# Optimization experiments

Hardware: AMD Instinct MI355X
Metric: run time of the kernel (lower is better)

Reference implementation:

```python
import jax, jax.numpy as jnp
import numpy as np


def _ste(x, q):
    # straight-through estimator: forward=q, backward=identity
    return x + jax.lax.stop_gradient(q - x)


def quant_act_int8(x, s):
    # Int8 per-tensor fake-quant: clamp(round(x/s), -128, 127) * s
    q = jnp.clip(jnp.round(x / s), -128.0, 127.0) * s
    return _ste(x, q)


def binarize_weight(w):
    # BINARY weight quant: scale * sign(w), scale = mean(|w|) per tensor (STE)
    s = jnp.mean(jnp.abs(jax.lax.stop_gradient(w)))
    return _ste(w, s * jnp.sign(w))


def setup_inputs() -> dict:
    key = jax.random.key(0)
    ks = jax.random.split(key, 7)
    B, D_IN, H, D_OUT = 65536, 784, 128, 10
    f32 = jnp.float32
    return {
        "input_tensor": jax.random.normal(ks[0], (B, D_IN), f32),
        "w1": jax.random.normal(ks[1], (D_IN, H), f32) * 0.05,
        "b1": jnp.zeros((H,), f32),
        "w2": jax.random.normal(ks[2], (H, H), f32) * 0.05,
        "b2": jnp.zeros((H,), f32),
        "w3": jax.random.normal(ks[3], (H, D_OUT), f32) * 0.05,
        "b3": jnp.zeros((D_OUT,), f32),
        # learned per-tensor activation scales (Int8ActPerTensorFloat)
        "s_in": jnp.float32(0.03),
        "s1i": jnp.float32(0.05), "s1o": jnp.float32(0.05),
        "s2i": jnp.float32(0.05), "s2o": jnp.float32(0.05),
        "s3i": jnp.float32(0.05), "s3o": jnp.float32(0.01),
    }


def reference(input_tensor, w1, b1, w2, b2, w3, b3,
              s_in, s1i, s1o, s2i, s2o, s3i, s3o):
    hidden = []
    # quantize_input (QuantIdentity, int8 per-tensor)
    x = quant_act_int8(input_tensor, s_in)
    hidden.append(x)
    # input_layer: binary QuantLinear + bias, then QuantReLU (input_quant + act_quant)
    x = x @ binarize_weight(w1) + b1
    x = quant_act_int8(x, s1i)
    x = quant_act_int8(jax.nn.relu(x), s1o)
    hidden.append(x)
    # hidden_layer
    x = x @ binarize_weight(w2) + b2
    x = quant_act_int8(x, s2i)
    x = quant_act_int8(jax.nn.relu(x), s2o)
    hidden.append(x)
    # output_layer: binary QuantLinear then QuantSigmoid
    x = x @ binarize_weight(w3) + b3
    x = quant_act_int8(x, s3i)
    x = quant_act_int8(jax.nn.sigmoid(x), s3o)
    hidden.append(x)
    return (x, *hidden)
```

## Files before the change

kernel.cpp:

```cpp
#include <hip/hip_runtime.h>
#include <math.h>

typedef __bf16 bf16x8 __attribute__((ext_vector_type(8)));
typedef float f32x4 __attribute__((ext_vector_type(4)));
typedef unsigned short u16;
typedef u16 u16x8 __attribute__((ext_vector_type(8)));

__device__ __forceinline__ float quantq_inv(float x, float inv) {
    return fminf(fmaxf(rintf(x * inv), -128.f), 127.f);
}

__device__ __forceinline__ u16 sign_bf16(float w) {
    return (w > 0.f) ? (u16)0x3F80 : ((w < 0.f) ? (u16)0xBF80 : (u16)0);
}

__global__ void alpha_part(const float* __restrict__ w1,
                           const float* __restrict__ w2,
                           const float* __restrict__ w3,
                           float* __restrict__ partial) {
    __shared__ float red[256];
    const int bid = blockIdx.x;
    const int m = bid >> 5, i = bid & 31;
    const float* w = (m == 0) ? w1 : ((m == 1) ? w2 : w3);
    const int n = (m == 0) ? 100352 : ((m == 1) ? 16384 : 1280);
    const int chunk = n >> 5;
    const float* p = w + i * chunk;
    float s = 0.f;
    for (int t = threadIdx.x; t < chunk; t += 256) s += fabsf(p[t]);
    red[threadIdx.x] = s;
    __syncthreads();
    for (int off = 128; off > 0; off >>= 1) {
        if ((int)threadIdx.x < off) red[threadIdx.x] += red[threadIdx.x + off];
        __syncthreads();
    }
    if (threadIdx.x == 0) partial[bid] = red[0];
}

__global__ void alpha_final(const float* __restrict__ partial,
                            float* __restrict__ alphas) {
    const int t = threadIdx.x;
    if (t < 3) {
        float s = 0.f;
        for (int i = 0; i < 32; ++i) s += partial[t * 32 + i];
        const int n = (t == 0) ? 100352 : ((t == 1) ? 16384 : 1280);
        alphas[t] = s / (float)n;
    }
}

__global__ void pack_kernel(const float* __restrict__ w1,
                            const float* __restrict__ w2,
                            const float* __restrict__ w3,
                            u16* __restrict__ Wb1) {
    u16* Wb2 = Wb1 + 102400;
    u16* Wb3 = Wb2 + 16384;
    int idx = blockIdx.x * 256 + threadIdx.x;
    if (idx < 102400) {
        int k = idx >> 7, n = idx & 127;
        u16 v = (k < 784) ? sign_bf16(w1[k * 128 + n]) : (u16)0;
        int dest = ((((k >> 5) * 8 + (n >> 4)) * 64) + ((((k & 31) >> 3) << 4) | (n & 15))) * 8 + (k & 7);
        Wb1[dest] = v;
    } else if (idx < 102400 + 16384) {
        int i = idx - 102400;
        int k = i >> 7, n = i & 127;
        u16 v = sign_bf16(w2[k * 128 + n]);
        int dest = ((((k >> 5) * 8 + (n >> 4)) * 64) + ((((k & 31) >> 3) << 4) | (n & 15))) * 8 + (k & 7);
        Wb2[dest] = v;
    } else if (idx < 102400 + 16384 + 2048) {
        int i = idx - 102400 - 16384;
        int k = i >> 4, n = i & 15;
        u16 v = (n < 10) ? sign_bf16(w3[k * 10 + n]) : (u16)0;
        int dest = (((k >> 5) * 64) + ((((k & 31) >> 3) << 4) | n)) * 8 + (k & 7);
        Wb3[dest] = v;
    }
}

__global__ __launch_bounds__(256) void fused_kernel(
    const float* __restrict__ input,
    const float* __restrict__ bias1, const float* __restrict__ bias2,
    const float* __restrict__ bias3,
    const float* __restrict__ ps_in, const float* __restrict__ ps1i,
    const float* __restrict__ ps1o, const float* __restrict__ ps2i,
    const float* __restrict__ ps2o, const float* __restrict__ ps3i,
    const float* __restrict__ ps3o,
    const float* __restrict__ alphas, const u16* __restrict__ Wb1,
    float* __restrict__ out0, float* __restrict__ h0, float* __restrict__ h1,
    float* __restrict__ h2, float* __restrict__ h3)
{
    const u16* Wb2 = Wb1 + 102400;
    const u16* Wb3 = Wb2 + 16384;

    __shared__ u16 A2[8192];

    const int tid = threadIdx.x;
    const int wave = tid >> 6, lane = tid & 63;
    const int row0 = blockIdx.x * 64;

    const float s_in = *ps_in, s1i = *ps1i, s1o = *ps1o;
    const float s2i = *ps2i, s2o = *ps2o, s3i = *ps3i, s3o = *ps3o;
    const float inv_sin = 1.f / s_in, inv_s1i = 1.f / s1i, inv_s1o = 1.f / s1o;
    const float inv_s2i = 1.f / s2i, inv_s2o = 1.f / s2o;
    const float inv_s3i = 1.f / s3i, inv_s3o = 1.f / s3o;
    const float alpha1 = alphas[0], alpha2 = alphas[1], alpha3 = alphas[2];

    const int rA = lane & 15;
    const int gA = lane >> 4;
    const size_t arow = (size_t)(row0 + wave * 16 + rA) * 784;

    f32x4 acc1[8];
#pragma unroll
    for (int n = 0; n < 8; ++n) acc1[n] = f32x4{0.f, 0.f, 0.f, 0.f};

    f32x4 pv0, pv1;
    {
        const float* p = input + arow + gA * 8;
        pv0 = *reinterpret_cast<const f32x4*>(p);
        pv1 = *reinterpret_cast<const f32x4*>(p + 4);
    }
    const u16* bw1 = Wb1 + (size_t)lane * 8;

    for (int ksq = 0; ksq < 25; ++ksq) {
        float v[8];
#pragma unroll
        for (int j = 0; j < 4; ++j) { v[j] = pv0[j]; v[4 + j] = pv1[j]; }
        const bool valid = (ksq < 24) || (gA < 2);

        if (ksq < 24) {
            const int cb = (ksq + 1) * 32 + gA * 8;
            if (cb + 8 <= 784) {
                const float* p = input + arow + cb;
                pv0 = *reinterpret_cast<const f32x4*>(p);
                pv1 = *reinterpret_cast<const f32x4*>(p + 4);
            }
        }

        u16x8 qb;
        if (valid) {
            float q[8];
#pragma unroll
            for (int j = 0; j < 8; ++j) q[j] = quantq_inv(v[j], inv_sin);
            f32x4 ha = {q[0] * s_in, q[1] * s_in, q[2] * s_in, q[3] * s_in};
            f32x4 hb = {q[4] * s_in, q[5] * s_in, q[6] * s_in, q[7] * s_in};
            float* hp = h0 + arow + ksq * 32 + gA * 8;
            __builtin_nontemporal_store(ha, reinterpret_cast<f32x4*>(hp));
            __builtin_nontemporal_store(hb, reinterpret_cast<f32x4*>(hp + 4));
#pragma unroll
            for (int j = 0; j < 8; ++j) qb[j] = (u16)(__float_as_uint(q[j]) >> 16);
        } else {
#pragma unroll
            for (int j = 0; j < 8; ++j) qb[j] = (u16)0;
        }
        union { u16x8 u; bf16x8 b; } cvt;
        cvt.u = qb;
        const bf16x8 a = cvt.b;

        const u16* bp = bw1 + (size_t)ksq * 4096;
#pragma unroll
        for (int n = 0; n < 8; ++n) {
            const bf16x8 b = *reinterpret_cast<const bf16x8*>(bp + n * 512);
            acc1[n] = __builtin_amdgcn_mfma_f32_16x16x32_bf16(a, b, acc1[n], 0, 0, 0);
        }
    }

    const int cl = lane & 15;
    const int rh = lane >> 4;
    {
        const float a1s = alpha1 * s_in;
#pragma unroll
        for (int n = 0; n < 8; ++n) {
            const int col = n * 16 + cl;
            const float bias = bias1[col];
            const int ks = n >> 1;
            const int gk = ((n & 1) * 2) + (cl >> 3);
            const int jd = cl & 7;
#pragma unroll
            for (int j = 0; j < 4; ++j) {
                const int rl = rh * 4 + j;
                float x = a1s * acc1[n][j] + bias;
                x = quantq_inv(x, inv_s1i) * s1i;
                x = fmaxf(x, 0.f);
                const float qv = quantq_inv(x, inv_s1o);
                __builtin_nontemporal_store(qv * s1o,
                    h1 + (size_t)(row0 + wave * 16 + rl) * 128 + col);
                A2[(((ks * 4 + wave) * 64) + (gk * 16 + rl)) * 8 + jd] =
                    (u16)(__float_as_uint(qv) >> 16);
            }
        }
    }

    f32x4 acc2[8];
#pragma unroll
    for (int n = 0; n < 8; ++n) acc2[n] = f32x4{0.f, 0.f, 0.f, 0.f};
#pragma unroll
    for (int ks = 0; ks < 4; ++ks) {
        const bf16x8 a = *reinterpret_cast<const bf16x8*>(&A2[((ks * 4 + wave) * 64 + lane) * 8]);
#pragma unroll
        for (int n = 0; n < 8; ++n) {
            const bf16x8 b = *reinterpret_cast<const bf16x8*>(Wb2 + ((size_t)(ks * 8 + n) * 64 + lane) * 8);
            acc2[n] = __builtin_amdgcn_mfma_f32_16x16x32_bf16(a, b, acc2[n], 0, 0, 0);
        }
    }

    {
        const float a2s = alpha2 * s1o;
#pragma unroll
        for (int n = 0; n < 8; ++n) {
            const int col = n * 16 + cl;
            const float bias = bias2[col];
            const int ks = n >> 1;
            const int gk = ((n & 1) * 2) + (cl >> 3);
            const int jd = cl & 7;
#pragma unroll
            for (int j = 0; j < 4; ++j) {
                const int rl = rh * 4 + j;
                float x = a2s * acc2[n][j] + bias;
                x = quantq_inv(x, inv_s2i) * s2i;
                x = fmaxf(x, 0.f);
                const float qv = quantq_inv(x, inv_s2o);
                __builtin_nontemporal_store(qv * s2o,
                    h2 + (size_t)(row0 + wave * 16 + rl) * 128 + col);
                A2[(((ks * 4 + wave) * 64) + (gk * 16 + rl)) * 8 + jd] =
                    (u16)(__float_as_uint(qv) >> 16);
            }
        }
    }

    f32x4 acc3 = f32x4{0.f, 0.f, 0.f, 0.f};
#pragma unroll
    for (int ks = 0; ks < 4; ++ks) {
        const bf16x8 a = *reinterpret_cast<const bf16x8*>(&A2[((ks * 4 + wave) * 64 + lane) * 8]);
        const bf16x8 b = *reinterpret_cast<const bf16x8*>(Wb3 + ((size_t)ks * 64 + lane) * 8);
        acc3 = __builtin_amdgcn_mfma_f32_16x16x32_bf16(a, b, acc3, 0, 0, 0);
    }

    if (cl < 10) {
        const float a3s = alpha3 * s2o;
        const float bias = bias3[cl];
#pragma unroll
        for (int j = 0; j < 4; ++j) {
            const int rgl = row0 + wave * 16 + rh * 4 + j;
            float x = a3s * acc3[j] + bias;
            x = quantq_inv(x, inv_s3i) * s3i;
            const float sg = 1.f / (1.f + expf(-x));
            const float qv = quantq_inv(sg, inv_s3o) * s3o;
            out0[(size_t)rgl * 10 + cl] = qv;
            h3[(size_t)rgl * 10 + cl] = qv;
        }
    }
}

extern "C" void kernel_launch(void* const* d_in, const int* in_sizes, int n_in,
                              void* d_out, int out_size, void* d_ws, size_t ws_size,
                              hipStream_t stream) {
    const float* input = (const float*)d_in[0];
    const float* w1    = (const float*)d_in[1];
    const float* bias1 = (const float*)d_in[2];
    const float* w2    = (const float*)d_in[3];
    const float* bias2 = (const float*)d_in[4];
    const float* w3    = (const float*)d_in[5];
    const float* bias3 = (const float*)d_in[6];
    const float* s_in  = (const float*)d_in[7];
    const float* s1i   = (const float*)d_in[8];
    const float* s1o   = (const float*)d_in[9];
    const float* s2i   = (const float*)d_in[10];
    const float* s2o   = (const float*)d_in[11];
    const float* s3i   = (const float*)d_in[12];
    const float* s3o   = (const float*)d_in[13];

    float* out = (float*)d_out;
    float* out0 = out;
    float* h0 = out + 655360;
    float* h1 = out + 52035584;
    float* h2 = out + 60424192;
    float* h3 = out + 68812800;

    float* alphas  = (float*)d_ws;
    float* partial = (float*)((char*)d_ws + 16);
    u16*   Wb1     = (u16*)((char*)d_ws + 512);

    alpha_part<<<96, 256, 0, stream>>>(w1, w2, w3, partial);
    alpha_final<<<1, 64, 0, stream>>>(partial, alphas);
    pack_kernel<<<472, 256, 0, stream>>>(w1, w2, w3, Wb1);
    fused_kernel<<<1024, 256, 0, stream>>>(input, bias1, bias2, bias3,
                                           s_in, s1i, s1o, s2i, s2o, s3i, s3o,
                                           alphas, Wb1,
                                           out0, h0, h1, h2, h3);
}
```

Before: 122.0 us.

## Split layer-1 K loop across two wave groups and merge alpha_final into pack

Doubles the fused kernel block to 512 threads. Two groups of four waves each handle half of the 784-wide K dimension of the first GEMM, with two-deep register prefetch of the input, and their partial accumulators are reduced through shared memory before the second half of the block exits. The goal is more memory-level parallelism and latency hiding on the input read, which dominates the kernel. The alpha_final launch is folded into pack_kernel to save one launch. The cost is extra shared memory, three block barriers, and half the threads sitting idle for layers 2 and 3.

```diff
diff --git a/kernel.cpp b/kernel.cpp
--- a/kernel.cpp
+++ b/kernel.cpp
@@ -36,21 +36,19 @@
     if (threadIdx.x == 0) partial[bid] = red[0];
 }
 
-__global__ void alpha_final(const float* __restrict__ partial,
+__global__ void pack_kernel(const float* __restrict__ w1,
+                            const float* __restrict__ w2,
+                            const float* __restrict__ w3,
+                            u16* __restrict__ Wb1,
+                            const float* __restrict__ partial,
                             float* __restrict__ alphas) {
-    const int t = threadIdx.x;
-    if (t < 3) {
+    if (blockIdx.x == 0 && threadIdx.x < 3) {
+        const int t = threadIdx.x;
         float s = 0.f;
         for (int i = 0; i < 32; ++i) s += partial[t * 32 + i];
         const int n = (t == 0) ? 100352 : ((t == 1) ? 16384 : 1280);
         alphas[t] = s / (float)n;
     }
-}
-
-__global__ void pack_kernel(const float* __restrict__ w1,
-                            const float* __restrict__ w2,
-                            const float* __restrict__ w3,
-                            u16* __restrict__ Wb1) {
     u16* Wb2 = Wb1 + 102400;
     u16* Wb3 = Wb2 + 16384;
     int idx = blockIdx.x * 256 + threadIdx.x;
@@ -74,7 +72,7 @@
     }
 }
 
-__global__ __launch_bounds__(256) void fused_kernel(
+__global__ __launch_bounds__(512, 8) void fused_kernel(
     const float* __restrict__ input,
     const float* __restrict__ bias1, const float* __restrict__ bias2,
     const float* __restrict__ bias3,
@@ -89,10 +87,12 @@
     const u16* Wb2 = Wb1 + 102400;
     const u16* Wb3 = Wb2 + 16384;
 
+    __shared__ f32x4 Xch[1024];
     __shared__ u16 A2[8192];
 
     const int tid = threadIdx.x;
     const int wave = tid >> 6, lane = tid & 63;
+    const int wq = wave & 3, khalf = wave >> 2;
     const int row0 = blockIdx.x * 64;
 
     const float s_in = *ps_in, s1i = *ps1i, s1o = *ps1o;
@@ -104,62 +104,105 @@
 
     const int rA = lane & 15;
     const int gA = lane >> 4;
-    const size_t arow = (size_t)(row0 + wave * 16 + rA) * 784;
+    const size_t arow = (size_t)(row0 + wq * 16 + rA) * 784;
+    const float* __restrict__ inA = input + arow + gA * 8;
+    float* __restrict__ h0A = h0 + arow + gA * 8;
+    const u16* bw1 = Wb1 + (size_t)lane * 8;
 
     f32x4 acc1[8];
 #pragma unroll
     for (int n = 0; n < 8; ++n) acc1[n] = f32x4{0.f, 0.f, 0.f, 0.f};
 
-    f32x4 pv0, pv1;
-    {
-        const float* p = input + arow + gA * 8;
-        pv0 = *reinterpret_cast<const f32x4*>(p);
-        pv1 = *reinterpret_cast<const f32x4*>(p + 4);
-    }
-    const u16* bw1 = Wb1 + (size_t)lane * 8;
-
-    for (int ksq = 0; ksq < 25; ++ksq) {
-        float v[8];
-#pragma unroll
-        for (int j = 0; j < 4; ++j) { v[j] = pv0[j]; v[4 + j] = pv1[j]; }
-        const bool valid = (ksq < 24) || (gA < 2);
-
-        if (ksq < 24) {
-            const int cb = (ksq + 1) * 32 + gA * 8;
-            if (cb + 8 <= 784) {
-                const float* p = input + arow + cb;
-                pv0 = *reinterpret_cast<const f32x4*>(p);
-                pv1 = *reinterpret_cast<const f32x4*>(p + 4);
-            }
-        }
-
-        u16x8 qb;
-        if (valid) {
-            float q[8];
-#pragma unroll
-            for (int j = 0; j < 8; ++j) q[j] = quantq_inv(v[j], inv_sin);
+    auto consume = [&](int ksq, f32x4 va, f32x4 vb, bool dostore) {
+        float q[8];
+#pragma unroll
+        for (int j = 0; j < 4; ++j) {
+            q[j]     = quantq_inv(va[j], inv_sin);
+            q[4 + j] = quantq_inv(vb[j], inv_sin);
+        }
+        if (dostore) {
             f32x4 ha = {q[0] * s_in, q[1] * s_in, q[2] * s_in, q[3] * s_in};
             f32x4 hb = {q[4] * s_in, q[5] * s_in, q[6] * s_in, q[7] * s_in};
-            float* hp = h0 + arow + ksq * 32 + gA * 8;
+            float* hp = h0A + ksq * 32;
             __builtin_nontemporal_store(ha, reinterpret_cast<f32x4*>(hp));
             __builtin_nontemporal_store(hb, reinterpret_cast<f32x4*>(hp + 4));
-#pragma unroll
-            for (int j = 0; j < 8; ++j) qb[j] = (u16)(__float_as_uint(q[j]) >> 16);
-        } else {
-#pragma unroll
-            for (int j = 0; j < 8; ++j) qb[j] = (u16)0;
-        }
+        }
+        u16x8 qb;
+#pragma unroll
+        for (int j = 0; j < 8; ++j) qb[j] = (u16)(__float_as_uint(q[j]) >> 16);
         union { u16x8 u; bf16x8 b; } cvt;
         cvt.u = qb;
         const bf16x8 a = cvt.b;
-
         const u16* bp = bw1 + (size_t)ksq * 4096;
 #pragma unroll
         for (int n = 0; n < 8; ++n) {
             const bf16x8 b = *reinterpret_cast<const bf16x8*>(bp + n * 512);
             acc1[n] = __builtin_amdgcn_mfma_f32_16x16x32_bf16(a, b, acc1[n], 0, 0, 0);
         }
-    }
+    };
+
+    if (khalf == 0) {
+        f32x4 pa = *reinterpret_cast<const f32x4*>(inA + 0);
+        f32x4 pb = *reinterpret_cast<const f32x4*>(inA + 4);
+        f32x4 qa = *reinterpret_cast<const f32x4*>(inA + 32);
+        f32x4 qb = *reinterpret_cast<const f32x4*>(inA + 36);
+#pragma unroll
+        for (int k = 0; k < 12; ++k) {
+            f32x4 na = pa, nb = pb;
+            if (k + 2 < 12) {
+                na = *reinterpret_cast<const f32x4*>(inA + (k + 2) * 32);
+                nb = *reinterpret_cast<const f32x4*>(inA + (k + 2) * 32 + 4);
+            }
+            consume(k, pa, pb, true);
+            pa = qa; pb = qb; qa = na; qb = nb;
+        }
+    } else {
+        f32x4 pa = *reinterpret_cast<const f32x4*>(inA + 12 * 32);
+        f32x4 pb = *reinterpret_cast<const f32x4*>(inA + 12 * 32 + 4);
+        f32x4 qa = *reinterpret_cast<const f32x4*>(inA + 13 * 32);
+        f32x4 qb = *reinterpret_cast<const f32x4*>(inA + 13 * 32 + 4);
+#pragma unroll
+        for (int k = 0; k < 13; ++k) {
+            const int ksq = 12 + k;
+            const int t = ksq + 2;
+            f32x4 na, nb;
+            if (t < 24) {
+                na = *reinterpret_cast<const f32x4*>(inA + t * 32);
+                nb = *reinterpret_cast<const f32x4*>(inA + t * 32 + 4);
+            } else if (t == 24) {
+                if (gA < 2) {
+                    na = *reinterpret_cast<const f32x4*>(inA + 768);
+                    nb = *reinterpret_cast<const f32x4*>(inA + 768 + 4);
+                } else {
+                    na = f32x4{0.f, 0.f, 0.f, 0.f};
+                    nb = f32x4{0.f, 0.f, 0.f, 0.f};
+                }
+            } else {
+                na = pa; nb = pb;
+            }
+            consume(ksq, pa, pb, (ksq < 24) || (gA < 2));
+            pa = qa; pb = qb; qa = na; qb = nb;
+        }
+    }
+
+    if (khalf == 1) {
+#pragma unroll
+        for (int n = 0; n < 4; ++n) Xch[(wq * 4 + n) * 64 + lane] = acc1[n];
+    }
+    __syncthreads();
+    if (khalf == 0) {
+#pragma unroll
+        for (int n = 0; n < 4; ++n) acc1[n] += Xch[(wq * 4 + n) * 64 + lane];
+    }
+    __syncthreads();
+    if (khalf == 1) {
+#pragma unroll
+        for (int n = 0; n < 4; ++n) Xch[(wq * 4 + n) * 64 + lane] = acc1[4 + n];
+    }
+    __syncthreads();
+    if (khalf == 1) return;
+#pragma unroll
+    for (int n = 0; n < 4; ++n) acc1[4 + n] += Xch[(wq * 4 + n) * 64 + lane];
 
     const int cl = lane & 15;
     const int rh = lane >> 4;
@@ -180,8 +223,8 @@
                 x = fmaxf(x, 0.f);
                 const float qv = quantq_inv(x, inv_s1o);
                 __builtin_nontemporal_store(qv * s1o,
-                    h1 + (size_t)(row0 + wave * 16 + rl) * 128 + col);
-                A2[(((ks * 4 + wave) * 64) + (gk * 16 + rl)) * 8 + jd] =
+                    h1 + (size_t)(row0 + wq * 16 + rl) * 128 + col);
+                A2[(((ks * 4 + wq) * 64) + (gk * 16 + rl)) * 8 + jd] =
                     (u16)(__float_as_uint(qv) >> 16);
             }
         }
@@ -192,7 +235,7 @@
     for (int n = 0; n < 8; ++n) acc2[n] = f32x4{0.f, 0.f, 0.f, 0.f};
 #pragma unroll
     for (int ks = 0; ks < 4; ++ks) {
-        const bf16x8 a = *reinterpret_cast<const bf16x8*>(&A2[((ks * 4 + wave) * 64 + lane) * 8]);
+        const bf16x8 a = *reinterpret_cast<const bf16x8*>(&A2[((ks * 4 + wq) * 64 + lane) * 8]);
 #pragma unroll
         for (int n = 0; n < 8; ++n) {
             const bf16x8 b = *reinterpret_cast<const bf16x8*>(Wb2 + ((size_t)(ks * 8 + n) * 64 + lane) * 8);
@@ -217,8 +260,8 @@
                 x = fmaxf(x, 0.f);
                 const float qv = quantq_inv(x, inv_s2o);
                 __builtin_nontemporal_store(qv * s2o,
-                    h2 + (size_t)(row0 + wave * 16 + rl) * 128 + col);
-                A2[(((ks * 4 + wave) * 64) + (gk * 16 + rl)) * 8 + jd] =
+                    h2 + (size_t)(row0 + wq * 16 + rl) * 128 + col);
+                A2[(((ks * 4 + wq) * 64) + (gk * 16 + rl)) * 8 + jd] =
                     (u16)(__float_as_uint(qv) >> 16);
             }
         }
@@ -227,7 +270,7 @@
     f32x4 acc3 = f32x4{0.f, 0.f, 0.f, 0.f};
 #pragma unroll
     for (int ks = 0; ks < 4; ++ks) {
-        const bf16x8 a = *reinterpret_cast<const bf16x8*>(&A2[((ks * 4 + wave) * 64 + lane) * 8]);
+        const bf16x8 a = *reinterpret_cast<const bf16x8*>(&A2[((ks * 4 + wq) * 64 + lane) * 8]);
         const bf16x8 b = *reinterpret_cast<const bf16x8*>(Wb3 + ((size_t)ks * 64 + lane) * 8);
         acc3 = __builtin_amdgcn_mfma_f32_16x16x32_bf16(a, b, acc3, 0, 0, 0);
     }
@@ -237,7 +280,7 @@
         const float bias = bias3[cl];
 #pragma unroll
         for (int j = 0; j < 4; ++j) {
-            const int rgl = row0 + wave * 16 + rh * 4 + j;
+            const int rgl = row0 + wq * 16 + rh * 4 + j;
             float x = a3s * acc3[j] + bias;
             x = quantq_inv(x, inv_s3i) * s3i;
             const float sg = 1.f / (1.f + expf(-x));
@@ -278,9 +321,8 @@
     u16*   Wb1     = (u16*)((char*)d_ws + 512);
 
     alpha_part<<<96, 256, 0, stream>>>(w1, w2, w3, partial);
-    alpha_final<<<1, 64, 0, stream>>>(partial, alphas);
-    pack_kernel<<<472, 256, 0, stream>>>(w1, w2, w3, Wb1);
-    fused_kernel<<<1024, 256, 0, stream>>>(input, bias1, bias2, bias3,
+    pack_kernel<<<472, 256, 0, stream>>>(w1, w2, w3, Wb1, partial, alphas);
+    fused_kernel<<<1024, 512, 0, stream>>>(input, bias1, bias2, bias3,
                                            s_in, s1i, s1o, s2i, s2o, s3i, s3o,
                                            alphas, Wb1,
                                            out0, h0, h1, h2, h3);
```

After: 335.9 us. 2.75x slower.
